# Performance work log

Hardware: AMD Instinct MI355X
Metric: run time of the kernel (lower is better)

Reference implementation:

```python
import jax, jax.numpy as jnp
import numpy as np

N = 50000
E = 800000
IN_DIM = 256
HID = 256
OUT_DIM = 2


def setup_inputs() -> dict:
    key = jax.random.key(0)
    ks = jax.random.split(key, 10)
    x = jax.random.normal(ks[0], (N, IN_DIM), dtype=jnp.float32)
    edge_index = jax.random.randint(ks[1], (2, E), 0, N, dtype=jnp.int64)
    # Glorot-ish scaling so activations stay well-conditioned through 4 layers
    def w(k, fan_in, fan_out):
        return jax.random.normal(k, (fan_in, fan_out), dtype=jnp.float32) / jnp.sqrt(jnp.float32(fan_in))
    return {
        "x": x,
        "edge_index": edge_index,
        "W0": w(ks[2], IN_DIM, HID), "b0": jnp.zeros((HID,), jnp.float32),
        "W1": w(ks[3], HID, HID),    "b1": jnp.zeros((HID,), jnp.float32),
        "W2": w(ks[4], HID, HID),    "b2": jnp.zeros((HID,), jnp.float32),
        "W3": w(ks[5], HID, OUT_DIM), "b3": jnp.zeros((OUT_DIM,), jnp.float32),
    }


def _gcn_norm(edge_index, n, dtype):
    # PyG gcn_norm with self-loops: deg over destination, norm = d^-1/2[src]*d^-1/2[dst]
    loops = jnp.arange(n, dtype=edge_index.dtype)
    src = jnp.concatenate([edge_index[0], loops])
    dst = jnp.concatenate([edge_index[1], loops])
    deg = jax.ops.segment_sum(jnp.ones_like(dst, dtype=dtype), dst, num_segments=n)
    dis = deg ** -0.5  # deg >= 1 due to self-loops
    norm = dis[src] * dis[dst]
    return src, dst, norm


def reference(x, edge_index, W0, b0, W1, b1, W2, b2, W3, b3):
    n = x.shape[0]
    src, dst, norm = _gcn_norm(edge_index, n, x.dtype)

    def conv(h, W, b):
        h = h @ W                              # [N, F_out] dense GEMM
        msg = h[src] * norm[:, None]           # edge-gather + scale
        agg = jax.ops.segment_sum(msg, dst, num_segments=n)  # scatter-add
        return agg + b

    h = jax.nn.relu(conv(x, W0, b0))
    h = jax.nn.relu(conv(h, W1, b1))
    h = jax.nn.relu(conv(h, W2, b2))
    return conv(h, W3, b3)
```

## Files before the change

kernel.cpp:

```cpp
#include <hip/hip_runtime.h>

#define N_NODES 50000
#define N_EDGES 800000

static inline int cdiv(int a, int b) { return (a + b - 1) / b; }

typedef __attribute__((ext_vector_type(8))) short bf16x8;
typedef __attribute__((ext_vector_type(4))) float f32x4;

static __device__ __forceinline__ unsigned short f2bf(float f) {
    unsigned int u = __float_as_uint(f);
    unsigned int r = (u + 0x7FFF + ((u >> 16) & 1)) >> 16;
    return (unsigned short)r;
}
static __device__ __forceinline__ float bf2f(unsigned short h) {
    return __uint_as_float((unsigned int)h << 16);
}
static __device__ __forceinline__ float bf_lo(unsigned int u) { return __uint_as_float(u << 16); }
static __device__ __forceinline__ float bf_hi(unsigned int u) { return __uint_as_float(u & 0xFFFF0000u); }

static __device__ __forceinline__ int logc(int p) {
    int pl = p & 63;
    return (p & ~63) + (pl & 3) * 16 + (pl >> 2);
}

static __device__ __forceinline__ void acc8(float* acc, uint4 v, float wgt) {
    acc[0] += wgt * bf_lo(v.x);
    acc[1] += wgt * bf_hi(v.x);
    acc[2] += wgt * bf_lo(v.y);
    acc[3] += wgt * bf_hi(v.y);
    acc[4] += wgt * bf_lo(v.z);
    acc[5] += wgt * bf_hi(v.z);
    acc[6] += wgt * bf_lo(v.w);
    acc[7] += wgt * bf_hi(v.w);
}


__global__ void k_count(const int* __restrict__ edst, int* cnt, int e) {
    int i = blockIdx.x * 256 + threadIdx.x;
    if (i < e) atomicAdd(&cnt[edst[i]], 1);
}

__global__ __launch_bounds__(256) void k_scan1(const int* __restrict__ cnt,
                                               int* __restrict__ row_ptr,
                                               float* __restrict__ dis,
                                               int* __restrict__ blk, int n) {
    __shared__ int sums[256];
    int t = threadIdx.x;
    int base = blockIdx.x * 1024 + t * 4;
    int c0 = 0, c1 = 0, c2 = 0, c3 = 0;
    if (base + 3 < n) {
        int4 v = *(const int4*)(cnt + base);
        c0 = v.x + 1; c1 = v.y + 1; c2 = v.z + 1; c3 = v.w + 1;
    } else {
        if (base + 0 < n) c0 = cnt[base + 0] + 1;
        if (base + 1 < n) c1 = cnt[base + 1] + 1;
        if (base + 2 < n) c2 = cnt[base + 2] + 1;
        if (base + 3 < n) c3 = cnt[base + 3] + 1;
    }
    int s = c0 + c1 + c2 + c3;
    sums[t] = s;
    __syncthreads();
    int x = s;
    for (int off = 1; off < 256; off <<= 1) {
        int y = (t >= off) ? sums[t - off] : 0;
        __syncthreads();
        x += y;
        sums[t] = x;
        __syncthreads();
    }
    int excl = x - s;
    if (base + 0 < n) { row_ptr[base + 0] = excl;                dis[base + 0] = rsqrtf((float)c0); }
    if (base + 1 < n) { row_ptr[base + 1] = excl + c0;           dis[base + 1] = rsqrtf((float)c1); }
    if (base + 2 < n) { row_ptr[base + 2] = excl + c0 + c1;      dis[base + 2] = rsqrtf((float)c2); }
    if (base + 3 < n) { row_ptr[base + 3] = excl + c0 + c1 + c2; dis[base + 3] = rsqrtf((float)c3); }
    if (t == 255) blk[blockIdx.x] = x;
}

__global__ __launch_bounds__(256) void k_scan2(int* __restrict__ blk,
                                               int* __restrict__ row_ptr_n, int nb) {
    __shared__ int sums[256];
    int t = threadIdx.x;
    int s = (t < nb) ? blk[t] : 0;
    sums[t] = s;
    __syncthreads();
    int x = s;
    for (int off = 1; off < 256; off <<= 1) {
        int y = (t >= off) ? sums[t - off] : 0;
        __syncthreads();
        x += y;
        sums[t] = x;
        __syncthreads();
    }
    if (t < nb) blk[t] = x - s;
    if (t == 255) row_ptr_n[0] = x;
}

__global__ __launch_bounds__(256) void k_scan3(int* __restrict__ row_ptr,
                                               int* __restrict__ pos,
                                               const int* __restrict__ blk, int n) {
    int base = blockIdx.x * 1024 + threadIdx.x * 4;
    int off = blk[blockIdx.x];
#pragma unroll
    for (int i = 0; i < 4; ++i) {
        int idx = base + i;
        if (idx < n) {
            int v = row_ptr[idx] + off;
            row_ptr[idx] = v;
            pos[idx] = v;
        }
    }
}

__global__ void k_fill(const int* __restrict__ esrc, const int* __restrict__ edst,
                       int* pos, const float* __restrict__ dis,
                       int2* __restrict__ eg, int e, int n) {
    int i = blockIdx.x * 256 + threadIdx.x;
    if (i < e) {
        int s = esrc[i], d = edst[i];
        int p = atomicAdd(&pos[d], 1);
        eg[p] = make_int2(s, __float_as_int(dis[s] * dis[d]));
    } else if (i < e + n) {
        int v = i - e;
        int p = atomicAdd(&pos[v], 1);
        float dv = dis[v];
        eg[p] = make_int2(v, __float_as_int(dv * dv));
    }
}


__global__ __launch_bounds__(256) void k_prep(const float* __restrict__ W0,
                                              const float* __restrict__ W1,
                                              const float* __restrict__ W2,
                                              unsigned short* __restrict__ Wth,
                                              unsigned short* __restrict__ Wtl,
                                              const float* __restrict__ X,
                                              unsigned short* __restrict__ Xh, long total4) {
    if (blockIdx.x < 768) {
        int layer = blockIdx.x >> 8;
        int n = blockIdx.x & 255;
        int p = threadIdx.x;
        const float* W = layer == 0 ? W0 : (layer == 1 ? W1 : W2);
        int k = (layer != 0) ? logc(p) : p;
        float v = W[(size_t)k * 256 + n];
        unsigned short h = f2bf(v);
        size_t o = (size_t)layer * 65536 + (size_t)n * 256 + p;
        Wth[o] = h;
        Wtl[o] = f2bf(v - bf2f(h));
    } else {
        long i = (long)(blockIdx.x - 768) * 256 + threadIdx.x;
        if (i >= total4) return;
        float4 v = *(const float4*)(X + i * 4);
        ushort4 h;
        h.x = f2bf(v.x);
        h.y = f2bf(v.y);
        h.z = f2bf(v.z);
        h.w = f2bf(v.w);
        *(ushort4*)(Xh + i * 4) = h;
    }
}


#define GEMM_RB 196

__global__ __launch_bounds__(256) void k_gemm_mfma(const unsigned short* __restrict__ Ah,
                                                   const unsigned short* __restrict__ Wth,
                                                   const unsigned short* __restrict__ Wtl,
                                                   unsigned short* __restrict__ C, int M) {
    __shared__ unsigned short Wh[64][264];
    __shared__ unsigned short Wl[64][264];
    int rowblk = blockIdx.x % GEMM_RB;
    int colblk = blockIdx.x / GEMM_RB;
    int c0 = colblk * 64;
    int m0 = rowblk * 256;
    int t = threadIdx.x;

    {
        int r = t >> 2;
        int k0 = (t & 3) * 64;
        const unsigned short* gh = Wth + (size_t)(c0 + r) * 256 + k0;
        const unsigned short* gl = Wtl + (size_t)(c0 + r) * 256 + k0;
        unsigned short* lh = &Wh[r][k0];
        unsigned short* ll = &Wl[r][k0];
#pragma unroll
        for (int i = 0; i < 8; ++i) {
            *(uint4*)(lh + i * 8) = *(const uint4*)(gh + i * 8);
            *(uint4*)(ll + i * 8) = *(const uint4*)(gl + i * 8);
        }
    }

    int lane = t & 63, wave = t >> 6;
    int quad = lane >> 4, l16 = lane & 15;

    const unsigned short* aph[4];
#pragma unroll
    for (int mt = 0; mt < 4; ++mt) {
        int m = m0 + wave * 64 + mt * 16 + l16;
        if (m >= M) m = M - 1;
        aph[mt] = Ah + (size_t)m * 256 + quad * 8;
    }

    bf16x8 ahf[4];
#pragma unroll
    for (int mt = 0; mt < 4; ++mt) ahf[mt] = *(const bf16x8*)(aph[mt]);

    __syncthreads();

    f32x4 acc[4][4];
#pragma unroll
    for (int i = 0; i < 4; ++i)
#pragma unroll
        for (int j = 0; j < 4; ++j) acc[i][j] = (f32x4){0.f, 0.f, 0.f, 0.f};

#pragma unroll
    for (int kc = 0; kc < 8; ++kc) {
        int ko = kc * 32 + quad * 8;
        bf16x8 nxt[4];
        if (kc < 7) {
#pragma unroll
            for (int mt = 0; mt < 4; ++mt) nxt[mt] = *(const bf16x8*)(aph[mt] + (kc + 1) * 32);
        }
#pragma unroll
        for (int nt = 0; nt < 4; ++nt) {
            bf16x8 bh = *(const bf16x8*)&Wh[nt * 16 + l16][ko];
            bf16x8 bl = *(const bf16x8*)&Wl[nt * 16 + l16][ko];
#pragma unroll
            for (int mt = 0; mt < 4; ++mt) {
                acc[mt][nt] = __builtin_amdgcn_mfma_f32_16x16x32_bf16(ahf[mt], bh, acc[mt][nt], 0, 0, 0);
                acc[mt][nt] = __builtin_amdgcn_mfma_f32_16x16x32_bf16(ahf[mt], bl, acc[mt][nt], 0, 0, 0);
            }
        }
        if (kc < 7) {
#pragma unroll
            for (int mt = 0; mt < 4; ++mt) ahf[mt] = nxt[mt];
        }
    }

#pragma unroll
    for (int mt = 0; mt < 4; ++mt) {
#pragma unroll
        for (int r = 0; r < 4; ++r) {
            int row = m0 + wave * 64 + mt * 16 + quad * 4 + r;
            if (row < M) {
                ushort4 sv;
                sv.x = f2bf(acc[mt][0][r]);
                sv.y = f2bf(acc[mt][1][r]);
                sv.z = f2bf(acc[mt][2][r]);
                sv.w = f2bf(acc[mt][3][r]);
                *(ushort4*)(C + (size_t)row * 256 + c0 + l16 * 4) = sv;
            }
        }
    }
}


__global__ __launch_bounds__(256) void k_agg256(const unsigned short* __restrict__ t,
                                                const int* __restrict__ row_ptr,
                                                const int2* __restrict__ eg,
                                                const float* __restrict__ bias,
                                                unsigned short* __restrict__ outh, int n) {
    int lane = threadIdx.x & 63;
    int wave = threadIdx.x >> 6;
    int node = blockIdx.x * 4 + wave;
    if (node >= n) return;
    int half = lane >> 5;
    int fl = lane & 31;
    int beg = row_ptr[node], end = row_ptr[node + 1];
    float acc[8] = {};
    const unsigned short* tp = t + fl * 8;

    int e = beg + half;
    for (; e + 6 < end; e += 8) {
        int2 a = eg[e], b = eg[e + 2], c = eg[e + 4], d = eg[e + 6];
        uint4 v0 = *(const uint4*)(tp + (size_t)a.x * 256);
        uint4 v1 = *(const uint4*)(tp + (size_t)b.x * 256);
        uint4 v2 = *(const uint4*)(tp + (size_t)c.x * 256);
        uint4 v3 = *(const uint4*)(tp + (size_t)d.x * 256);
        acc8(acc, v0, __int_as_float(a.y));
        acc8(acc, v1, __int_as_float(b.y));
        acc8(acc, v2, __int_as_float(c.y));
        acc8(acc, v3, __int_as_float(d.y));
    }
    for (; e + 2 < end; e += 4) {
        int2 a = eg[e], b = eg[e + 2];
        uint4 v0 = *(const uint4*)(tp + (size_t)a.x * 256);
        uint4 v1 = *(const uint4*)(tp + (size_t)b.x * 256);
        acc8(acc, v0, __int_as_float(a.y));
        acc8(acc, v1, __int_as_float(b.y));
    }
    if (e < end) {
        int2 a = eg[e];
        uint4 v0 = *(const uint4*)(tp + (size_t)a.x * 256);
        acc8(acc, v0, __int_as_float(a.y));
    }

#pragma unroll
    for (int i = 0; i < 8; ++i) acc[i] += __shfl_xor(acc[i], 32);

    if (half == 0) {
        ushort4 h0, h1;
#pragma unroll
        for (int j = 0; j < 8; ++j) {
            int cb = logc(fl * 8 + j);
            float v = acc[j] + bias[cb];
            v = v > 0.f ? v : 0.f;
            unsigned short h = f2bf(v);
            if (j == 0) h0.x = h;
            else if (j == 1) h0.y = h;
            else if (j == 2) h0.z = h;
            else if (j == 3) h0.w = h;
            else if (j == 4) h1.x = h;
            else if (j == 5) h1.y = h;
            else if (j == 6) h1.z = h;
            else h1.w = h;
        }
        unsigned short* oh = outh + (size_t)node * 256 + fl * 8;
        *(ushort4*)(oh + 0) = h0;
        *(ushort4*)(oh + 4) = h1;
    }
}


__global__ __launch_bounds__(256) void k_gemm_out2(const unsigned short* __restrict__ Hh,
                                                   const float* __restrict__ W3,
                                                   float* __restrict__ t2, int n) {
    int lane = threadIdx.x & 63;
    int wave = threadIdx.x >> 6;
    int row = blockIdx.x * 4 + wave;
    if (row >= n) return;
    ushort4 ah = *(const ushort4*)(Hh + (size_t)row * 256 + lane * 4);
    float v[4];
    v[0] = bf2f(ah.x);
    v[1] = bf2f(ah.y);
    v[2] = bf2f(ah.z);
    v[3] = bf2f(ah.w);
    float s0 = 0.f, s1 = 0.f;
#pragma unroll
    for (int i = 0; i < 4; ++i) {
        int c = logc(lane * 4 + i);
        float2 w = *(const float2*)(W3 + (size_t)c * 2);
        s0 += v[i] * w.x;
        s1 += v[i] * w.y;
    }
#pragma unroll
    for (int off = 32; off > 0; off >>= 1) {
        s0 += __shfl_down(s0, off);
        s1 += __shfl_down(s1, off);
    }
    if (lane == 0) {
        t2[(size_t)row * 2 + 0] = s0;
        t2[(size_t)row * 2 + 1] = s1;
    }
}

__global__ void k_agg2(const float* __restrict__ t2,
                       const int* __restrict__ row_ptr,
                       const int2* __restrict__ eg,
                       const float* __restrict__ b3,
                       float* __restrict__ out, int n) {
    int node = blockIdx.x * 256 + threadIdx.x;
    if (node >= n) return;
    int beg = row_ptr[node], end = row_ptr[node + 1];
    float a0 = 0.f, a1 = 0.f;
    for (int e = beg; e < end; ++e) {
        int2 m = eg[e];
        float w = __int_as_float(m.y);
        float2 v = *(const float2*)(t2 + (size_t)m.x * 2);
        a0 += w * v.x;
        a1 += w * v.y;
    }
    out[(size_t)node * 2 + 0] = a0 + b3[0];
    out[(size_t)node * 2 + 1] = a1 + b3[1];
}


extern "C" void kernel_launch(void* const* d_in, const int* in_sizes, int n_in,
                              void* d_out, int out_size, void* d_ws, size_t ws_size,
                              hipStream_t stream) {
    const int N = N_NODES, E = N_EDGES;
    const float* x  = (const float*)d_in[0];
    const int* ei   = (const int*)d_in[1];
    const int* esrc = ei;
    const int* edst = ei + E;
    const float* W0 = (const float*)d_in[2];
    const float* b0 = (const float*)d_in[3];
    const float* W1 = (const float*)d_in[4];
    const float* b1 = (const float*)d_in[5];
    const float* W2 = (const float*)d_in[6];
    const float* b2 = (const float*)d_in[7];
    const float* W3 = (const float*)d_in[8];
    const float* b3 = (const float*)d_in[9];
    float* out = (float*)d_out;

    unsigned short* Ahh = (unsigned short*)d_ws;
    unsigned short* Tb  = Ahh + (size_t)N * 256;
    unsigned short* Wth = Tb + (size_t)N * 256;
    unsigned short* Wtl = Wth + 3 * 65536;
    int2*  eg     = (int2*)(Wtl + 3 * 65536);
    float* t2     = (float*)(eg + (E + N));
    float* dis    = t2 + (size_t)N * 2;
    int*   cnt    = (int*)(dis + N);
    int*   row_ptr= cnt + N;
    int*   pos    = row_ptr + (N + 1);
    int*   blk    = pos + N;

    const int NB = cdiv(N, 1024);

    hipMemsetAsync(cnt, 0, (size_t)N * sizeof(int), stream);
    k_count<<<cdiv(E, 256), 256, 0, stream>>>(edst, cnt, E);
    k_scan1<<<NB, 256, 0, stream>>>(cnt, row_ptr, dis, blk, N);
    k_scan2<<<1, 256, 0, stream>>>(blk, row_ptr + N, NB);
    k_scan3<<<NB, 256, 0, stream>>>(row_ptr, pos, blk, N);
    k_fill<<<cdiv(E + N, 256), 256, 0, stream>>>(esrc, edst, pos, dis, eg, E, N);

    const int ggrid = GEMM_RB * 4;
    const int agrid = cdiv(N, 4);
    const long total4 = (long)N * 64;
    const int CA = cdiv((int)total4, 256);

    k_prep<<<768 + CA, 256, 0, stream>>>(W0, W1, W2, Wth, Wtl, x, Ahh, total4);

    k_gemm_mfma<<<ggrid, 256, 0, stream>>>(Ahh, Wth, Wtl, Tb, N);
    k_agg256<<<agrid, 256, 0, stream>>>(Tb, row_ptr, eg, b0, Ahh, N);
    k_gemm_mfma<<<ggrid, 256, 0, stream>>>(Ahh, Wth + 65536, Wtl + 65536, Tb, N);
    k_agg256<<<agrid, 256, 0, stream>>>(Tb, row_ptr, eg, b1, Ahh, N);
    k_gemm_mfma<<<ggrid, 256, 0, stream>>>(Ahh, Wth + 2 * 65536, Wtl + 2 * 65536, Tb, N);
    k_agg256<<<agrid, 256, 0, stream>>>(Tb, row_ptr, eg, b2, Ahh, N);
    k_gemm_out2<<<agrid, 256, 0, stream>>>(Ahh, W3, t2, N);
    k_agg2<<<cdiv(N, 256), 256, 0, stream>>>(t2, row_ptr, eg, b3, out, N);
}
```

Before: 480.6 us.

## Split hi/lo weight passes to halve GEMM shared memory and drop A prefetch

The GEMM now keeps one 64x264 shared tile instead of separate hi and lo weight tiles. It loads the hi part, runs a full K pass, then reloads the tile with the lo part and runs a second K pass. The explicit A-fragment register prefetch is removed and the K loop is only partially unrolled. The aim is less LDS and register pressure per block so more blocks can be resident. The cost is that the A operand is read from global memory twice, with extra barriers and less latency hiding inside each pass.

```diff
diff --git a/kernel.cpp b/kernel.cpp
--- a/kernel.cpp
+++ b/kernel.cpp
@@ -167,27 +167,14 @@
                                                    const unsigned short* __restrict__ Wth,
                                                    const unsigned short* __restrict__ Wtl,
                                                    unsigned short* __restrict__ C, int M) {
-    __shared__ unsigned short Wh[64][264];
-    __shared__ unsigned short Wl[64][264];
+    __shared__ unsigned short Wb[64][264];
     int rowblk = blockIdx.x % GEMM_RB;
     int colblk = blockIdx.x / GEMM_RB;
     int c0 = colblk * 64;
     int m0 = rowblk * 256;
     int t = threadIdx.x;
-
-    {
-        int r = t >> 2;
-        int k0 = (t & 3) * 64;
-        const unsigned short* gh = Wth + (size_t)(c0 + r) * 256 + k0;
-        const unsigned short* gl = Wtl + (size_t)(c0 + r) * 256 + k0;
-        unsigned short* lh = &Wh[r][k0];
-        unsigned short* ll = &Wl[r][k0];
-#pragma unroll
-        for (int i = 0; i < 8; ++i) {
-            *(uint4*)(lh + i * 8) = *(const uint4*)(gh + i * 8);
-            *(uint4*)(ll + i * 8) = *(const uint4*)(gl + i * 8);
-        }
-    }
+    int sr = t >> 2;
+    int sk0 = (t & 3) * 64;
 
     int lane = t & 63, wave = t >> 6;
     int quad = lane >> 4, l16 = lane & 15;
@@ -200,39 +187,56 @@
         aph[mt] = Ah + (size_t)m * 256 + quad * 8;
     }
 
-    bf16x8 ahf[4];
-#pragma unroll
-    for (int mt = 0; mt < 4; ++mt) ahf[mt] = *(const bf16x8*)(aph[mt]);
-
+    f32x4 acc[4][4];
+#pragma unroll
+    for (int i = 0; i < 4; ++i)
+#pragma unroll
+        for (int j = 0; j < 4; ++j) acc[i][j] = (f32x4){0.f, 0.f, 0.f, 0.f};
+
+    {
+        const unsigned short* gh = Wth + (size_t)(c0 + sr) * 256 + sk0;
+        unsigned short* lh = &Wb[sr][sk0];
+#pragma unroll
+        for (int i = 0; i < 8; ++i)
+            *(uint4*)(lh + i * 8) = *(const uint4*)(gh + i * 8);
+    }
     __syncthreads();
-
-    f32x4 acc[4][4];
-#pragma unroll
-    for (int i = 0; i < 4; ++i)
-#pragma unroll
-        for (int j = 0; j < 4; ++j) acc[i][j] = (f32x4){0.f, 0.f, 0.f, 0.f};
-
-#pragma unroll
+#pragma unroll 2
     for (int kc = 0; kc < 8; ++kc) {
-        int ko = kc * 32 + quad * 8;
-        bf16x8 nxt[4];
-        if (kc < 7) {
-#pragma unroll
-            for (int mt = 0; mt < 4; ++mt) nxt[mt] = *(const bf16x8*)(aph[mt] + (kc + 1) * 32);
+        int ko = kc * 32;
+        bf16x8 ahf[4];
+#pragma unroll
+        for (int mt = 0; mt < 4; ++mt) ahf[mt] = *(const bf16x8*)(aph[mt] + ko);
+#pragma unroll
+        for (int nt = 0; nt < 4; ++nt) {
+            bf16x8 bh = *(const bf16x8*)&Wb[nt * 16 + l16][ko + quad * 8];
+#pragma unroll
+            for (int mt = 0; mt < 4; ++mt)
+                acc[mt][nt] = __builtin_amdgcn_mfma_f32_16x16x32_bf16(ahf[mt], bh, acc[mt][nt], 0, 0, 0);
         }
+    }
+    __syncthreads();
+
+    {
+        const unsigned short* gl = Wtl + (size_t)(c0 + sr) * 256 + sk0;
+        unsigned short* ll = &Wb[sr][sk0];
+#pragma unroll
+        for (int i = 0; i < 8; ++i)
+            *(uint4*)(ll + i * 8) = *(const uint4*)(gl + i * 8);
+    }
+    __syncthreads();
+#pragma unroll 2
+    for (int kc = 0; kc < 8; ++kc) {
+        int ko = kc * 32;
+        bf16x8 ahf[4];
+#pragma unroll
+        for (int mt = 0; mt < 4; ++mt) ahf[mt] = *(const bf16x8*)(aph[mt] + ko);
 #pragma unroll
         for (int nt = 0; nt < 4; ++nt) {
-            bf16x8 bh = *(const bf16x8*)&Wh[nt * 16 + l16][ko];
-            bf16x8 bl = *(const bf16x8*)&Wl[nt * 16 + l16][ko];
-#pragma unroll
-            for (int mt = 0; mt < 4; ++mt) {
-                acc[mt][nt] = __builtin_amdgcn_mfma_f32_16x16x32_bf16(ahf[mt], bh, acc[mt][nt], 0, 0, 0);
+            bf16x8 bl = *(const bf16x8*)&Wb[nt * 16 + l16][ko + quad * 8];
+#pragma unroll
+            for (int mt = 0; mt < 4; ++mt)
                 acc[mt][nt] = __builtin_amdgcn_mfma_f32_16x16x32_bf16(ahf[mt], bl, acc[mt][nt], 0, 0, 0);
-            }
-        }
-        if (kc < 7) {
-#pragma unroll
-            for (int mt = 0; mt < 4; ++mt) ahf[mt] = nxt[mt];
         }
     }
 
```

After: 514.6 us. 1.07x slower.
